# Kernel tuning notes

Hardware: AMD Instinct MI355X
Metric: run time of the kernel (lower is better)

Reference implementation:

```python
import jax, jax.numpy as jnp
import numpy as np

B, C, H, W = 512, 3, 64, 32
K = 2                      # fractional pool kernel size
HOUT, WOUT = 38, 16        # floor(64*0.6), floor(32*0.5)
HID = 128                  # RNN hidden size
D = C * HOUT               # RNN input size = 114


def _frac_starts(in_size, out_size, k, u=0.5):
    # PyTorch fractional-max-pool interval formula with deterministic sample u
    alpha = (in_size - k) / (out_size - 1)
    i = np.arange(out_size - 1)
    starts = np.floor((i + u) * alpha) - np.floor(u * alpha)
    return np.concatenate([starts, [in_size - k]]).astype(np.int32)

ROW = _frac_starts(H, HOUT, K)   # (HOUT,) window start rows
COL = _frac_starts(W, WOUT, K)   # (WOUT,) window start cols


def setup_inputs() -> dict:
    key = jax.random.key(0)
    ks = jax.random.split(key, 5)
    s = 1.0 / np.sqrt(HID)  # torch RNNCell init scale
    return {
        "x": jax.random.normal(ks[0], (B, C, H, W), jnp.float32),
        "W_ih": jax.random.uniform(ks[1], (HID, D), jnp.float32, -s, s),
        "W_hh": jax.random.uniform(ks[2], (HID, HID), jnp.float32, -s, s),
        "b_ih": jax.random.uniform(ks[3], (HID,), jnp.float32, -s, s),
        "b_hh": jax.random.uniform(ks[4], (HID,), jnp.float32, -s, s),
    }


def reference(x, W_ih, W_hh, b_ih, b_hh):
    # 1) fractional max pool, kernel 2: pairwise max over gathered window starts
    xr = jnp.maximum(x[:, :, ROW, :], x[:, :, ROW + 1, :])          # (B,C,HOUT,W)
    pooled = jnp.maximum(xr[:, :, :, COL], xr[:, :, :, COL + 1])    # (B,C,HOUT,WOUT)
    # 2) exact (erf-based) GELU, matching torch nn.GELU default
    act = jax.nn.gelu(pooled, approximate=False)
    # 3) sequence over width: (WOUT, B, C*HOUT), C-major flatten matches torch view
    seq = act.transpose(3, 0, 1, 2).reshape(WOUT, B, D)
    # 4) vanilla RNNCell across time via scan
    def step(h, xt):
        h = jnp.tanh(xt @ W_ih.T + b_ih + h @ W_hh.T + b_hh)
        return h, h
    _, outs = jax.lax.scan(step, jnp.zeros((B, HID), x.dtype), seq)  # (WOUT,B,HID)
    # 5) temporal mean + tanh
    t_mean = jnp.tanh(outs.mean(axis=0))                             # (B,HID)
    # 6) modulate by global spatial mean of pooled; torch broadcasting of
    #    (B,HID) * (B,1,1,1) yields (B,1,B,HID) — replicated faithfully
    s_mean = pooled.mean(axis=(1, 2, 3), keepdims=True)              # (B,1,1,1)
    return t_mean * s_mean                                           # (B,1,B,HID)
```

## Files before the change

### kernel.cpp

```cpp
#include <hip/hip_runtime.h>
#include <math.h>

#define BB   512
#define CC   3
#define HH   64
#define WW   32
#define HOUT 38
#define WOUT 16
#define HID  128
#define DD   114
#define SEQQ 36
#define SEQP 144
#define WIHP 132
#define WHHP 132
#define NPOOL (CC*HOUT*WOUT)

typedef float f32x4 __attribute__((ext_vector_type(4)));

__device__ __forceinline__ float fast_tanh(float u) {
    return 1.f - 2.f / (__expf(2.f * u) + 1.f);
}

#define WS_SMEAN 0
#define WS_TMEAN 512

__global__ __launch_bounds__(512, 4)
void k1_fused(const float* __restrict__ x,
              const float* __restrict__ Wih,
              const float* __restrict__ Whh,
              const float* __restrict__ bih,
              const float* __restrict__ bhh,
              float* __restrict__ s_mean,
              float* __restrict__ t_mean)
{
    __shared__ __align__(16) float wst[HID * WHHP];
    __shared__ __align__(16) float seq[WOUT][SEQP];
    __shared__ __align__(16) float hbuf[2][SEQP];
    __shared__ float red[8];
    __shared__ int   rowl[HOUT];

    const int tid  = threadIdx.x;
    const int wid  = tid >> 6;
    const int lane = tid & 63;
    const int kl   = (wid << 4) | (lane & 15);
    const int kc   = lane >> 4;
    const int b    = blockIdx.x;

    f32x4 xpf[3];
    {
        const f32x4* xg = (const f32x4*)(x + (size_t)b * (CC*HH*WW));
        #pragma unroll
        for (int i = 0; i < 3; ++i) xpf[i] = xg[tid + 512*i];
    }
    f32x4 wihpf[7], wihtail;
    {
        const f32x4* wg = (const f32x4*)Wih;
        #pragma unroll
        for (int i = 0; i < 7; ++i) wihpf[i] = wg[tid + 512*i];
        if (tid < 64) wihtail = wg[3584 + tid];
    }

    if (tid < HOUT) {
        double alpha = (double)(HH - 2) / (double)(HOUT - 1);
        rowl[tid] = (tid < HOUT - 1)
            ? (int)(floor((tid + 0.5) * alpha) - floor(0.5 * alpha))
            : (HH - 2);
    }
    if (tid < HID) hbuf[0][SEQQ*(tid >> 5) + (tid & 31)] = 0.f;
    if (tid < 224) {
        int t = tid / 14, o = 18 + tid % 14;
        seq[t][3*SEQQ + o] = 0.f;
    }

    {
        f32x4* xd = (f32x4*)wst;
        #pragma unroll
        for (int i = 0; i < 3; ++i) xd[tid + 512*i] = xpf[i];
    }
    __syncthreads();

    float ps = 0.f;
    #pragma unroll
    for (int it = 0; it < 4; ++it) {
        int idx = tid + it*512;
        if (idx < NPOOL) {
            int c  = idx / (HOUT*WOUT);
            int r  = idx % (HOUT*WOUT);
            int ho = r / WOUT;
            int wo = r % WOUT;
            const float* p0 = &wst[c*(HH*WW) + rowl[ho]*WW + 2*wo];
            float m = fmaxf(fmaxf(p0[0], p0[1]), fmaxf(p0[WW], p0[WW+1]));
            ps += m;
            int d = c*HOUT + ho;
            seq[wo][SEQQ*(d >> 5) + (d & 31)] =
                0.5f * m * (1.f + erff(m * 0.70710678118654752440f));
        }
    }
    #pragma unroll
    for (int off = 32; off > 0; off >>= 1) ps += __shfl_down(ps, off);
    if (lane == 0) red[wid] = ps;
    __syncthreads();
    if (tid == 0) {
        float r = 0.f;
        #pragma unroll
        for (int i = 0; i < 8; ++i) r += red[i];
        s_mean[b] = r * (1.f / (float)NPOOL);
    }

    #pragma unroll
    for (int i = 0; i < 7; ++i) {
        int j = 4*(tid + 512*i);
        #pragma unroll
        for (int e = 0; e < 4; ++e) {
            int r  = (j + e) / DD;
            int cc = (j + e) - r*DD;
            wst[r*WIHP + cc] = wihpf[i][e];
        }
    }
    if (tid < 64) {
        int j = 4*(3584 + tid);
        #pragma unroll
        for (int e = 0; e < 4; ++e) {
            int r  = (j + e) / DD;
            int cc = (j + e) - r*DD;
            wst[r*WIHP + cc] = wihtail[e];
        }
    }
    for (int j = tid; j < HID*14; j += 512)
        wst[(j/14)*WIHP + DD + (j % 14)] = 0.f;
    __syncthreads();

    f32x4 wih[8];
    {
        const f32x4* wr = (const f32x4*)&wst[kl*WIHP + (kc << 5)];
        #pragma unroll
        for (int dd = 0; dd < 8; ++dd) wih[dd] = wr[dd];
    }

    f32x4 whhpf[8];
    {
        const f32x4* hg = (const f32x4*)Whh;
        #pragma unroll
        for (int i = 0; i < 8; ++i) whhpf[i] = hg[tid + 512*i];
    }

    float zreg[WOUT];
    #pragma unroll
    for (int t = 0; t < WOUT; ++t) {
        const f32x4* a4 = (const f32x4*)&seq[t][kc*SEQQ];
        float s0 = 0.f, s1 = 0.f, s2 = 0.f, s3 = 0.f;
        #pragma unroll
        for (int dd = 0; dd < 8; ++dd) {
            f32x4 a = a4[dd], w = wih[dd];
            s0 = fmaf(w.x, a.x, s0);
            s1 = fmaf(w.y, a.y, s1);
            s2 = fmaf(w.z, a.z, s2);
            s3 = fmaf(w.w, a.w, s3);
        }
        float p = (s0 + s1) + (s2 + s3);
        p += __shfl_xor(p, 16);
        zreg[t] = p + __shfl_xor(p, 32);
    }
    {
        const float bias = bih[kl] + bhh[kl];
        #pragma unroll
        for (int t = 0; t < WOUT; ++t) zreg[t] += bias;
    }
    __syncthreads();

    #pragma unroll
    for (int i = 0; i < 8; ++i) {
        int j4 = tid + 512*i;
        *(f32x4*)&wst[(j4 >> 5)*WHHP + ((j4 & 31) << 2)] = whhpf[i];
    }
    __syncthreads();
    f32x4 whh[8];
    {
        const f32x4* wr = (const f32x4*)&wst[kl*WHHP + (kc << 5)];
        #pragma unroll
        for (int dd = 0; dd < 8; ++dd) whh[dd] = wr[dd];
    }

    float hsum = 0.f;
    #pragma unroll
    for (int t = 0; t < WOUT; ++t) {
        const int cur = t & 1, nxt = cur ^ 1;
        const f32x4* h4 = (const f32x4*)&hbuf[cur][kc*SEQQ];
        float s0 = 0.f, s1 = 0.f, s2 = 0.f, s3 = 0.f;
        #pragma unroll
        for (int dd = 0; dd < 8; ++dd) {
            f32x4 hv = h4[dd], w = whh[dd];
            s0 = fmaf(w.x, hv.x, s0);
            s1 = fmaf(w.y, hv.y, s1);
            s2 = fmaf(w.z, hv.z, s2);
            s3 = fmaf(w.w, hv.w, s3);
        }
        float p = (s0 + s1) + (s2 + s3);
        p += __shfl_xor(p, 16);
        float u  = zreg[t] + p + __shfl_xor(p, 32);
        float hn = fast_tanh(u);
        hsum += hn;
        if (kc == 0) hbuf[nxt][SEQQ*(kl >> 5) + (kl & 31)] = hn;
        __syncthreads();
    }
    if (kc == 0) t_mean[b*HID + kl] = fast_tanh(hsum * (1.f / 16.f));
}

__global__ __launch_bounds__(256)
void k2_out(const float* __restrict__ s_mean,
            const float* __restrict__ t_mean,
            f32x4* __restrict__ out)
{
    const int i   = blockIdx.x >> 3;
    const int sub = blockIdx.x & 7;
    const float s = s_mean[i];
    const f32x4* t4 = (const f32x4*)t_mean + sub*2048;
    f32x4*       o  = out + (size_t)i*16384 + sub*2048;
    const int tid = threadIdx.x;
    #pragma unroll
    for (int j = 0; j < 8; ++j) {
        int idx = tid + j*256;
        o[idx] = s * t4[idx];
    }
}

extern "C" void kernel_launch(void* const* d_in, const int* in_sizes, int n_in,
                              void* d_out, int out_size, void* d_ws, size_t ws_size,
                              hipStream_t stream)
{
    const float* x   = (const float*)d_in[0];
    const float* Wih = (const float*)d_in[1];
    const float* Whh = (const float*)d_in[2];
    const float* bih = (const float*)d_in[3];
    const float* bhh = (const float*)d_in[4];

    float* ws     = (float*)d_ws;
    float* s_mean = ws + WS_SMEAN;
    float* t_mean = ws + WS_TMEAN;

    k1_fused<<<dim3(BB), dim3(512), 0, stream>>>(x, Wih, Whh, bih, bhh, s_mean, t_mean);
    k2_out  <<<dim3(4096), dim3(256), 0, stream>>>(s_mean, t_mean, (f32x4*)d_out);
}
```

Baseline: 48.48 us.

## Fuse output broadcast into main kernel via grid-wide atomic counter barrier

Removes the second kernel and the t_mean round-trip through global memory. Each block publishes its spatial mean and bumps a global atomic counter, then spins until all blocks have done so. It then writes its own t_mean row times every block's s_mean directly into the output. This saves a kernel launch and a read pass, but adds a memset launch and a spin-wait that depends on all 512 blocks being co-resident. If they are not, the bounded spin can time out and produce wrong results.

After: 176.3 us. 264% more time.

```diff
diff --git a/kernel.cpp b/kernel.cpp
--- a/kernel.cpp
+++ b/kernel.cpp
@@ -21,17 +21,17 @@
     return 1.f - 2.f / (__expf(2.f * u) + 1.f);
 }
 
-#define WS_SMEAN 0
-#define WS_TMEAN 512
+#define WS_CNT_OFF 2048
 
 __global__ __launch_bounds__(512, 4)
-void k1_fused(const float* __restrict__ x,
-              const float* __restrict__ Wih,
-              const float* __restrict__ Whh,
-              const float* __restrict__ bih,
-              const float* __restrict__ bhh,
-              float* __restrict__ s_mean,
-              float* __restrict__ t_mean)
+void k_fused(const float* __restrict__ x,
+             const float* __restrict__ Wih,
+             const float* __restrict__ Whh,
+             const float* __restrict__ bih,
+             const float* __restrict__ bhh,
+             float* __restrict__ s_mean,
+             int*   __restrict__ bar_cnt,
+             f32x4* __restrict__ out)
 {
     __shared__ __align__(16) float wst[HID * WHHP];
     __shared__ __align__(16) float seq[WOUT][SEQP];
@@ -105,6 +105,9 @@
         #pragma unroll
         for (int i = 0; i < 8; ++i) r += red[i];
         s_mean[b] = r * (1.f / (float)NPOOL);
+        __threadfence();
+        __hip_atomic_fetch_add(bar_cnt, 1, __ATOMIC_RELEASE,
+                               __HIP_MEMORY_SCOPE_AGENT);
     }
 
     #pragma unroll
@@ -203,24 +206,30 @@
         if (kc == 0) hbuf[nxt][SEQQ*(kl >> 5) + (kl & 31)] = hn;
         __syncthreads();
     }
-    if (kc == 0) t_mean[b*HID + kl] = fast_tanh(hsum * (1.f / 16.f));
-}
-
-__global__ __launch_bounds__(256)
-void k2_out(const float* __restrict__ s_mean,
-            const float* __restrict__ t_mean,
-            f32x4* __restrict__ out)
-{
-    const int i   = blockIdx.x >> 3;
-    const int sub = blockIdx.x & 7;
-    const float s = s_mean[i];
-    const f32x4* t4 = (const f32x4*)t_mean + sub*2048;
-    f32x4*       o  = out + (size_t)i*16384 + sub*2048;
-    const int tid = threadIdx.x;
-    #pragma unroll
-    for (int j = 0; j < 8; ++j) {
-        int idx = tid + j*256;
-        o[idx] = s * t4[idx];
+    if (kc == 0) hbuf[0][kl] = fast_tanh(hsum * (1.f / 16.f));
+
+    if (tid == 0) {
+        int iters = 0;
+        while (__hip_atomic_load(bar_cnt, __ATOMIC_ACQUIRE,
+                                 __HIP_MEMORY_SCOPE_AGENT) < BB
+               && iters < 5000000) {
+            __builtin_amdgcn_s_sleep(2);
+            ++iters;
+        }
+    }
+    __syncthreads();
+    __threadfence();
+
+    {
+        const int col  = tid & 31;
+        const int isub = tid >> 5;
+        const f32x4 tm = *(const f32x4*)&hbuf[0][col << 2];
+        f32x4* ob = out + (size_t)b * 32;
+        #pragma unroll
+        for (int p = 0; p < 32; ++p) {
+            int i = (p << 4) + isub;
+            ob[(size_t)i * 16384 + col] = s_mean[i] * tm;
+        }
     }
 }
 
@@ -234,10 +243,10 @@
     const float* bih = (const float*)d_in[3];
     const float* bhh = (const float*)d_in[4];
 
-    float* ws     = (float*)d_ws;
-    float* s_mean = ws + WS_SMEAN;
-    float* t_mean = ws + WS_TMEAN;
-
-    k1_fused<<<dim3(BB), dim3(512), 0, stream>>>(x, Wih, Whh, bih, bhh, s_mean, t_mean);
-    k2_out  <<<dim3(4096), dim3(256), 0, stream>>>(s_mean, t_mean, (f32x4*)d_out);
+    float* s_mean  = (float*)d_ws;
+    int*   bar_cnt = (int*)((char*)d_ws + WS_CNT_OFF);
+
+    hipMemsetAsync(bar_cnt, 0, sizeof(int), stream);
+    k_fused<<<dim3(BB), dim3(512), 0, stream>>>(
+        x, Wih, Whh, bih, bhh, s_mean, bar_cnt, (f32x4*)d_out);
 }
```
